# Performance work log

Hardware: AMD Instinct MI355X
Metric: run time of the kernel (lower is better)

Reference implementation:

```python
import jax, jax.numpy as jnp
import numpy as np

EPS = 1e-12
NUM_KNOTS = 30


def _pchip_slopes(y, x):
    """Shape-preserving PCHIP slopes at knots. y,x: [K], K>2, x strictly increasing."""
    h = x[1:] - x[:-1]                      # [K-1]
    delta = (y[1:] - y[:-1]) / (h + EPS)    # [K-1]
    hkm1, hk = h[:-1], h[1:]
    w1 = 2.0 * hk + hkm1
    w2 = hk + 2.0 * hkm1
    same_sign = delta[:-1] * delta[1:] > 0
    d_int = (w1 + w2) / (w1 / (delta[:-1] + EPS) + w2 / (delta[1:] + EPS))
    d_mid = jnp.where(same_sign, d_int, jnp.zeros_like(d_int))  # [K-2]
    # one-sided endpoint slopes with monotonicity limiting
    d0 = ((2.0 * h[0] + h[1]) * delta[0] - h[0] * delta[1]) / (h[0] + h[1] + EPS)
    dN = ((2.0 * h[-1] + h[-2]) * delta[-1] - h[-1] * delta[-2]) / (h[-1] + h[-2] + EPS)

    def _limit(di, de):
        di = jnp.where(di * de <= 0, jnp.zeros_like(di), di)
        return jnp.where(jnp.abs(di) > 3.0 * jnp.abs(de), 3.0 * de, di)

    d0 = _limit(d0, delta[0])
    dN = _limit(dN, delta[-1])
    return jnp.concatenate([d0[None], d_mid, dN[None]])  # [K]


def setup_inputs() -> dict:
    key = jax.random.key(0)
    k1, k2 = jax.random.split(key)
    x = jax.random.uniform(k1, (8192, 4096), dtype=jnp.float32)  # inputs inside knot domain [0,1)
    knots = jnp.linspace(0.0, 1.0, NUM_KNOTS, dtype=jnp.float32)  # buffer: uniform knots
    coeffs = jax.random.normal(k2, (NUM_KNOTS,), dtype=jnp.float32) * 0.5  # learned knot values
    return {"x": x, "knots": knots, "coeffs": coeffs}


def reference(x, knots, coeffs):
    """PCHIP cubic Hermite spline evaluated elementwise at x."""
    K = knots.shape[0]
    d = _pchip_slopes(coeffs, knots)
    xc = jnp.clip(x, knots[0], knots[-1])
    idx = jnp.clip(jnp.searchsorted(knots, xc) - 1, 0, K - 2)
    xk, xk1 = knots[idx], knots[idx + 1]
    yk, yk1 = coeffs[idx], coeffs[idx + 1]
    dk, dk1 = d[idx], d[idx + 1]
    h = xk1 - xk
    safe_h = jnp.where(jnp.abs(h) < EPS, jnp.ones_like(h), h)
    t = jnp.where(jnp.abs(h) < EPS, jnp.zeros_like(xc), (xc - xk) / safe_h)
    t2 = t * t
    t3 = t2 * t
    h00 = 2.0 * t3 - 3.0 * t2 + 1.0
    h10 = t3 - 2.0 * t2 + t
    h01 = -2.0 * t3 + 3.0 * t2
    h11 = t3 - t2
    return h00 * yk + h10 * safe_h * dk + h01 * yk1 + h11 * safe_h * dk1
```

## Files before the change

kernel.cpp:

```cpp
#include <hip/hip_runtime.h>

#define EPSF 1e-12f
#define NKNOTS 30
#define NINT 29

typedef float fvec4 __attribute__((ext_vector_type(4)));


__global__ __launch_bounds__(256) void SimpleSpline_kernel(
    const float* __restrict__ x,
    const float* __restrict__ knots,
    const float* __restrict__ coeffs,
    float* __restrict__ out,
    int n)
{
    __shared__ fvec4 cf[NINT];
    __shared__ float dsh[NKNOTS];

    const int tid = threadIdx.x;

    if (tid < NKNOTS) {
        float d;
        if (tid == 0) {
            float h0 = knots[1] - knots[0];
            float h1 = knots[2] - knots[1];
            float de0 = (coeffs[1] - coeffs[0]) / (h0 + EPSF);
            float de1 = (coeffs[2] - coeffs[1]) / (h1 + EPSF);
            d = ((2.0f * h0 + h1) * de0 - h0 * de1) / (h0 + h1 + EPSF);
            if (d * de0 <= 0.0f) d = 0.0f;
            if (fabsf(d) > 3.0f * fabsf(de0)) d = 3.0f * de0;
        } else if (tid == NKNOTS - 1) {
            float hN = knots[NKNOTS - 1] - knots[NKNOTS - 2];
            float hM = knots[NKNOTS - 2] - knots[NKNOTS - 3];
            float deN = (coeffs[NKNOTS - 1] - coeffs[NKNOTS - 2]) / (hN + EPSF);
            float deM = (coeffs[NKNOTS - 2] - coeffs[NKNOTS - 3]) / (hM + EPSF);
            d = ((2.0f * hN + hM) * deN - hN * deM) / (hN + hM + EPSF);
            if (d * deN <= 0.0f) d = 0.0f;
            if (fabsf(d) > 3.0f * fabsf(deN)) d = 3.0f * deN;
        } else {
            float hkm1 = knots[tid] - knots[tid - 1];
            float hk   = knots[tid + 1] - knots[tid];
            float dkm1 = (coeffs[tid] - coeffs[tid - 1]) / (hkm1 + EPSF);
            float dk   = (coeffs[tid + 1] - coeffs[tid]) / (hk + EPSF);
            float w1 = 2.0f * hk + hkm1;
            float w2 = hk + 2.0f * hkm1;
            d = 0.0f;
            if (dkm1 * dk > 0.0f)
                d = (w1 + w2) / (w1 / (dkm1 + EPSF) + w2 / (dk + EPSF));
        }
        dsh[tid] = d;
    }
    __syncthreads();

    if (tid < NINT) {
        float h = knots[tid + 1] - knots[tid];
        float safe_h = (fabsf(h) < EPSF) ? 1.0f : h;
        float yk  = coeffs[tid];
        float yk1 = coeffs[tid + 1];
        float sdk  = safe_h * dsh[tid];
        float sdk1 = safe_h * dsh[tid + 1];
        fvec4 c;
        c.x = yk;
        c.y = sdk;
        c.z = 3.0f * (yk1 - yk) - 2.0f * sdk - sdk1;
        c.w = 2.0f * (yk - yk1) + sdk + sdk1;
        cf[tid] = c;
    }
    __syncthreads();

    auto eval1 = [&](float xi) -> float {
        float s = fminf(fmaxf(xi * 29.0f, 0.0f), 29.0f);
        int idx = (int)s;
        idx = idx > (NINT - 1) ? (NINT - 1) : idx;
        float t = s - (float)idx;
        fvec4 c = cf[idx];
        return fmaf(t, fmaf(t, fmaf(t, c.w, c.z), c.y), c.x);
    };

    const int n4 = n >> 2;
    const int stride = gridDim.x * blockDim.x;
    const fvec4* __restrict__ xv = (const fvec4*)x;
    fvec4* __restrict__ ov = (fvec4*)out;

    for (int i = blockIdx.x * blockDim.x + tid; i < n4; i += stride) {
        fvec4 v = xv[i];
        fvec4 r;
        r.x = eval1(v.x);
        r.y = eval1(v.y);
        r.z = eval1(v.z);
        r.w = eval1(v.w);
        __builtin_nontemporal_store(r, &ov[i]);
    }

    const int rem = n & 3;
    if (rem) {
        const int base = n4 << 2;
        const int g = blockIdx.x * blockDim.x + tid;
        if (g < rem) out[base + g] = eval1(x[base + g]);
    }
}

extern "C" void kernel_launch(void* const* d_in, const int* in_sizes, int n_in,
                              void* d_out, int out_size, void* d_ws, size_t ws_size,
                              hipStream_t stream) {
    const float* x      = (const float*)d_in[0];
    const float* knots  = (const float*)d_in[1];
    const float* coeffs = (const float*)d_in[2];
    float* out = (float*)d_out;
    const int n = in_sizes[0];

    const int block = 256;
    int n4 = n >> 2;
    int blocks = (n4 + block - 1) / block;
    if (blocks > 2048) blocks = 2048;
    if (blocks < 1) blocks = 1;

    SimpleSpline_kernel<<<blocks, block, 0, stream>>>(x, knots, coeffs, out, n);
}
```

Before: 235.0 us.

## Software-pipeline grid-stride loop with batched prefetch of next input vectors

Restructures the grid-stride loop so each thread loads BATCH float4 vectors ahead, then computes and stores the current batch while the next batch's loads are in flight. This is meant to raise memory-level parallelism and hide global load latency in a bandwidth-bound elementwise kernel. It costs extra registers for the double buffer, which may lower occupancy.

```diff
diff --git a/kernel.cpp b/kernel.cpp
--- a/kernel.cpp
+++ b/kernel.cpp
@@ -3,6 +3,7 @@
 #define EPSF 1e-12f
 #define NKNOTS 30
 #define NINT 29
+#define BATCH 4
 
 typedef float fvec4 __attribute__((ext_vector_type(4)));
 
@@ -79,24 +80,53 @@
 
     const int n4 = n >> 2;
     const int stride = gridDim.x * blockDim.x;
+    const int i0 = blockIdx.x * blockDim.x + tid;
     const fvec4* __restrict__ xv = (const fvec4*)x;
     fvec4* __restrict__ ov = (fvec4*)out;
 
-    for (int i = blockIdx.x * blockDim.x + tid; i < n4; i += stride) {
-        fvec4 v = xv[i];
-        fvec4 r;
-        r.x = eval1(v.x);
-        r.y = eval1(v.y);
-        r.z = eval1(v.z);
-        r.w = eval1(v.w);
-        __builtin_nontemporal_store(r, &ov[i]);
+    fvec4 v[BATCH];
+    int cn = 0;
+    int base = i0;
+
+    #pragma unroll
+    for (int b = 0; b < BATCH; ++b) {
+        int j = base + b * stride;
+        if (j < n4) { v[b] = xv[j]; cn = b + 1; }
+    }
+
+    while (cn > 0) {
+        const int nbase = base + BATCH * stride;
+
+        fvec4 w[BATCH];
+        int wn = 0;
+        #pragma unroll
+        for (int b = 0; b < BATCH; ++b) {
+            int j = nbase + b * stride;
+            if (j < n4) { w[b] = xv[j]; wn = b + 1; }
+        }
+
+        #pragma unroll
+        for (int b = 0; b < BATCH; ++b) {
+            if (b < cn) {
+                fvec4 r;
+                r.x = eval1(v[b].x);
+                r.y = eval1(v[b].y);
+                r.z = eval1(v[b].z);
+                r.w = eval1(v[b].w);
+                __builtin_nontemporal_store(r, &ov[base + b * stride]);
+            }
+        }
+
+        #pragma unroll
+        for (int b = 0; b < BATCH; ++b) v[b] = w[b];
+        cn = wn;
+        base = nbase;
     }
 
     const int rem = n & 3;
     if (rem) {
-        const int base = n4 << 2;
-        const int g = blockIdx.x * blockDim.x + tid;
-        if (g < rem) out[base + g] = eval1(x[base + g]);
+        const int tbase = n4 << 2;
+        if (i0 < rem) out[tbase + i0] = eval1(x[tbase + i0]);
     }
 }
 
```

Result: slower. 240.0 us (+2.1%).

## Precompute spline coefficient table in a setup kernel and issue input load before barrier

Applied to the files above, without the earlier changes.

Moves the PCHIP slope and cubic coefficient computation into a single-block setup kernel that writes a small table to workspace. The main kernel now runs one element-vector per thread with no grid-stride loop and an uncapped grid, and issues its global input load before copying the table into shared memory. It also drops the nontemporal store hint. The aim is to hide load latency behind the per-block setup and barrier and to remove the redundant per-block slope math, at the cost of an extra kernel launch and many more short-lived blocks.

```diff
diff --git a/kernel.cpp b/kernel.cpp
--- a/kernel.cpp
+++ b/kernel.cpp
@@ -7,16 +7,12 @@
 typedef float fvec4 __attribute__((ext_vector_type(4)));
 
 
-__global__ __launch_bounds__(256) void SimpleSpline_kernel(
-    const float* __restrict__ x,
+__global__ __launch_bounds__(64) void spline_setup_kernel(
     const float* __restrict__ knots,
     const float* __restrict__ coeffs,
-    float* __restrict__ out,
-    int n)
+    fvec4* __restrict__ cft)
 {
-    __shared__ fvec4 cf[NINT];
     __shared__ float dsh[NKNOTS];
-
     const int tid = threadIdx.x;
 
     if (tid < NKNOTS) {
@@ -64,8 +60,27 @@
         c.y = sdk;
         c.z = 3.0f * (yk1 - yk) - 2.0f * sdk - sdk1;
         c.w = 2.0f * (yk - yk1) + sdk + sdk1;
-        cf[tid] = c;
-    }
+        cft[tid] = c;
+    }
+}
+
+__global__ __launch_bounds__(256) void SimpleSpline_kernel(
+    const float* __restrict__ x,
+    const fvec4* __restrict__ cft,
+    float* __restrict__ out,
+    int n)
+{
+    __shared__ fvec4 cf[NINT];
+
+    const int tid = threadIdx.x;
+    const int n4 = n >> 2;
+    const int gi = blockIdx.x * blockDim.x + tid;
+
+    const fvec4* __restrict__ xv = (const fvec4*)x;
+    int gil = gi < n4 ? gi : (n4 > 0 ? n4 - 1 : 0);
+    fvec4 v = xv[gil];
+
+    if (tid < NINT) cf[tid] = cft[tid];
     __syncthreads();
 
     auto eval1 = [&](float xi) -> float {
@@ -77,26 +92,106 @@
         return fmaf(t, fmaf(t, fmaf(t, c.w, c.z), c.y), c.x);
     };
 
-    const int n4 = n >> 2;
-    const int stride = gridDim.x * blockDim.x;
-    const fvec4* __restrict__ xv = (const fvec4*)x;
-    fvec4* __restrict__ ov = (fvec4*)out;
-
-    for (int i = blockIdx.x * blockDim.x + tid; i < n4; i += stride) {
-        fvec4 v = xv[i];
+    if (gi < n4) {
         fvec4 r;
         r.x = eval1(v.x);
         r.y = eval1(v.y);
         r.z = eval1(v.z);
         r.w = eval1(v.w);
-        __builtin_nontemporal_store(r, &ov[i]);
+        ((fvec4*)out)[gi] = r;
     }
 
     const int rem = n & 3;
     if (rem) {
-        const int base = n4 << 2;
-        const int g = blockIdx.x * blockDim.x + tid;
-        if (g < rem) out[base + g] = eval1(x[base + g]);
+        const int tbase = n4 << 2;
+        if (gi < rem) out[tbase + gi] = eval1(x[tbase + gi]);
+    }
+}
+
+__global__ __launch_bounds__(256) void SimpleSpline_kernel_self(
+    const float* __restrict__ x,
+    const float* __restrict__ knots,
+    const float* __restrict__ coeffs,
+    float* __restrict__ out,
+    int n)
+{
+    __shared__ fvec4 cf[NINT];
+    __shared__ float dsh[NKNOTS];
+    const int tid = threadIdx.x;
+
+    if (tid < NKNOTS) {
+        float d;
+        if (tid == 0) {
+            float h0 = knots[1] - knots[0];
+            float h1 = knots[2] - knots[1];
+            float de0 = (coeffs[1] - coeffs[0]) / (h0 + EPSF);
+            float de1 = (coeffs[2] - coeffs[1]) / (h1 + EPSF);
+            d = ((2.0f * h0 + h1) * de0 - h0 * de1) / (h0 + h1 + EPSF);
+            if (d * de0 <= 0.0f) d = 0.0f;
+            if (fabsf(d) > 3.0f * fabsf(de0)) d = 3.0f * de0;
+        } else if (tid == NKNOTS - 1) {
+            float hN = knots[NKNOTS - 1] - knots[NKNOTS - 2];
+            float hM = knots[NKNOTS - 2] - knots[NKNOTS - 3];
+            float deN = (coeffs[NKNOTS - 1] - coeffs[NKNOTS - 2]) / (hN + EPSF);
+            float deM = (coeffs[NKNOTS - 2] - coeffs[NKNOTS - 3]) / (hM + EPSF);
+            d = ((2.0f * hN + hM) * deN - hN * deM) / (hN + hM + EPSF);
+            if (d * deN <= 0.0f) d = 0.0f;
+            if (fabsf(d) > 3.0f * fabsf(deN)) d = 3.0f * deN;
+        } else {
+            float hkm1 = knots[tid] - knots[tid - 1];
+            float hk   = knots[tid + 1] - knots[tid];
+            float dkm1 = (coeffs[tid] - coeffs[tid - 1]) / (hkm1 + EPSF);
+            float dk   = (coeffs[tid + 1] - coeffs[tid]) / (hk + EPSF);
+            float w1 = 2.0f * hk + hkm1;
+            float w2 = hk + 2.0f * hkm1;
+            d = 0.0f;
+            if (dkm1 * dk > 0.0f)
+                d = (w1 + w2) / (w1 / (dkm1 + EPSF) + w2 / (dk + EPSF));
+        }
+        dsh[tid] = d;
+    }
+    __syncthreads();
+
+    if (tid < NINT) {
+        float h = knots[tid + 1] - knots[tid];
+        float safe_h = (fabsf(h) < EPSF) ? 1.0f : h;
+        float yk  = coeffs[tid];
+        float yk1 = coeffs[tid + 1];
+        float sdk  = safe_h * dsh[tid];
+        float sdk1 = safe_h * dsh[tid + 1];
+        fvec4 c;
+        c.x = yk;
+        c.y = sdk;
+        c.z = 3.0f * (yk1 - yk) - 2.0f * sdk - sdk1;
+        c.w = 2.0f * (yk - yk1) + sdk + sdk1;
+        cf[tid] = c;
+    }
+    __syncthreads();
+
+    auto eval1 = [&](float xi) -> float {
+        float s = fminf(fmaxf(xi * 29.0f, 0.0f), 29.0f);
+        int idx = (int)s;
+        idx = idx > (NINT - 1) ? (NINT - 1) : idx;
+        float t = s - (float)idx;
+        fvec4 c = cf[idx];
+        return fmaf(t, fmaf(t, fmaf(t, c.w, c.z), c.y), c.x);
+    };
+
+    const int n4 = n >> 2;
+    const int gi = blockIdx.x * blockDim.x + tid;
+    if (gi < n4) {
+        fvec4 v = ((const fvec4*)x)[gi];
+        fvec4 r;
+        r.x = eval1(v.x);
+        r.y = eval1(v.y);
+        r.z = eval1(v.z);
+        r.w = eval1(v.w);
+        ((fvec4*)out)[gi] = r;
+    }
+    const int rem = n & 3;
+    if (rem) {
+        const int tbase = n4 << 2;
+        if (gi < rem) out[tbase + gi] = eval1(x[tbase + gi]);
     }
 }
 
@@ -112,8 +207,13 @@
     const int block = 256;
     int n4 = n >> 2;
     int blocks = (n4 + block - 1) / block;
-    if (blocks > 2048) blocks = 2048;
     if (blocks < 1) blocks = 1;
 
-    SimpleSpline_kernel<<<blocks, block, 0, stream>>>(x, knots, coeffs, out, n);
-}
+    if (d_ws != nullptr && ws_size >= NINT * sizeof(fvec4)) {
+        fvec4* cft = (fvec4*)d_ws;
+        spline_setup_kernel<<<1, 64, 0, stream>>>(knots, coeffs, cft);
+        SimpleSpline_kernel<<<blocks, block, 0, stream>>>(x, cft, out, n);
+    } else {
+        SimpleSpline_kernel_self<<<blocks, block, 0, stream>>>(x, knots, coeffs, out, n);
+    }
+}
```

New measurement: 224.4 us. -4.5%, faster.
